# Kernel tuning notes

Measured on AMD Instinct MI355X. Metric: run time of the kernel, lower is better.

Reference implementation:

```python
import jax, jax.numpy as jnp
import numpy as np

DIM = 1024
NUM_HEADS = 16
HEAD_DIM = DIM // NUM_HEADS


def setup_inputs() -> dict:
    key = jax.random.key(0)
    ks = jax.random.split(key, 9)
    s = 1.0 / np.sqrt(DIM)
    return {
        "x": jax.random.normal(ks[0], (2, 2048, DIM), dtype=jnp.float32),
        "wq": jax.random.uniform(ks[1], (DIM, DIM), jnp.float32, -s, s),
        "bq": jax.random.uniform(ks[2], (DIM,), jnp.float32, -s, s),
        "wk": jax.random.uniform(ks[3], (DIM, DIM), jnp.float32, -s, s),
        "bk": jax.random.uniform(ks[4], (DIM,), jnp.float32, -s, s),
        "wv": jax.random.uniform(ks[5], (DIM, DIM), jnp.float32, -s, s),
        "bv": jax.random.uniform(ks[6], (DIM,), jnp.float32, -s, s),
        "wo": jax.random.uniform(ks[7], (DIM, DIM), jnp.float32, -s, s),
        "bo": jax.random.uniform(ks[8], (DIM,), jnp.float32, -s, s),
    }


def reference(x, wq, bq, wk, bk, wv, bv, wo, bo):
    B, N, D = x.shape
    H, Hd = NUM_HEADS, HEAD_DIM
    # projections; weights stored as (in, out) so x @ w matches torch Linear(x) with w = W.T
    q = (x @ wq + bq).reshape(B, N, H, Hd).transpose(0, 2, 1, 3)  # [B,H,N,Hd]
    k = (x @ wk + bk).reshape(B, N, H, Hd).transpose(0, 2, 1, 3)
    v = (x @ wv + bv).reshape(B, N, H, Hd).transpose(0, 2, 1, 3)
    scale = 1.0 / np.sqrt(Hd).astype(np.float32)
    scores = jnp.einsum("bhqd,bhkd->bhqk", q, k) * scale  # [B,H,N,N]
    attn = jax.nn.softmax(scores, axis=-1)
    # dropout is identity in eval mode (reference baseline)
    out = jnp.einsum("bhqk,bhkd->bhqd", attn, v)  # [B,H,N,Hd]
    out = out.transpose(0, 2, 1, 3).reshape(B, N, D)
    return out @ wo + bo
```

## Files before the change

kernel.cpp:

```cpp
#include <hip/hip_runtime.h>

typedef __attribute__((ext_vector_type(8))) short short8;
typedef __attribute__((ext_vector_type(4))) short short4v;
typedef __attribute__((ext_vector_type(4))) float f32x4;

__device__ inline unsigned short f2bf(float f) {
  union { float f; unsigned int u; } v; v.f = f;
  unsigned int r = v.u + 0x7FFFu + ((v.u >> 16) & 1u);
  return (unsigned short)(r >> 16);
}

__device__ inline unsigned cvtpk_bf16(float lo, float hi) {
  unsigned r;
  asm("v_cvt_pk_bf16_f32 %0, %1, %2" : "=v"(r) : "v"(lo), "v"(hi));
  return r;
}

__device__ inline void gload_lds16(const void* g, void* l) {
  __builtin_amdgcn_global_load_lds(
      (const __attribute__((address_space(1))) unsigned int*)g,
      (__attribute__((address_space(3))) unsigned int*)l, 16, 0, 0);
}


__global__ __launch_bounds__(256) void prep(
    const float* __restrict__ x,
    const float* __restrict__ wq, const float* __restrict__ wk,
    const float* __restrict__ wv, const float* __restrict__ wo,
    const float* __restrict__ bq, const float* __restrict__ bk,
    const float* __restrict__ bv,
    unsigned short* __restrict__ xb, unsigned short* __restrict__ wqkvT,
    unsigned short* __restrict__ woT, float* __restrict__ bqkv) {
  const int bid = blockIdx.x;
  if (bid < 4096) {
    const int i = bid * 256 + threadIdx.x;
    float4 v = ((const float4*)x)[i];
    ushort4 o;
    o.x = f2bf(v.x); o.y = f2bf(v.y); o.z = f2bf(v.z); o.w = f2bf(v.w);
    ((ushort4*)xb)[i] = o;
  } else if (bid < 8192) {
    const int u = bid - 4096;
    const int z = u >> 10, rem = u & 1023;
    const float* w = (z == 0) ? wq : (z == 1) ? wk : (z == 2) ? wv : wo;
    unsigned short* dst = (z < 3) ? (wqkvT + (size_t)z * 1024 * 1024) : woT;
    const float scale = (z == 0) ? 0.18033688011f : 1.0f;
    __shared__ float t[32][33];
    const int k0 = (rem & 31) * 32;
    const int n0 = (rem >> 5) * 32;
    const int tx = threadIdx.x & 31, ty = threadIdx.x >> 5;
#pragma unroll
    for (int i = 0; i < 32; i += 8)
      t[ty + i][tx] = w[(size_t)(k0 + ty + i) * 1024 + n0 + tx];
    __syncthreads();
#pragma unroll
    for (int i = 0; i < 32; i += 8)
      dst[(size_t)(n0 + ty + i) * 1024 + k0 + tx] = f2bf(t[tx][ty + i] * scale);
  } else {
    const int i = (bid - 8192) * 256 + threadIdx.x;
    float v;
    if (i < 1024) v = bq[i] * 0.18033688011f;
    else if (i < 2048) v = bk[i - 1024];
    else v = bv[i - 2048];
    bqkv[i] = v;
  }
}


__global__ __launch_bounds__(256) void gemm_bt64(
    const unsigned short* __restrict__ A, const unsigned short* __restrict__ Bt,
    const float* __restrict__ bias, float* __restrict__ C, int K, int ldc) {
  __shared__ unsigned short As[64 * 32];
  __shared__ unsigned short Bs[128 * 32];
  const int tid = threadIdx.x;
  const int lane = tid & 63;
  const int wave = tid >> 6;
  const int wm = (wave >> 1) * 32;
  const int wn = (wave & 1) * 64;
  const long bm = (long)blockIdx.x * 64;
  const long bn = (long)blockIdx.y * 128;

  const int sr = tid >> 2;
  const int sc = (tid & 3) * 8;
  const unsigned short* Ag0 = A + (bm + sr) * (long)K + sc;
  const unsigned short* Bg0 = Bt + (bn + sr) * (long)K + sc;
  const unsigned short* Bg1 = Bt + (bn + 64 + sr) * (long)K + sc;
  unsigned short* As0 = &As[tid * 8];
  unsigned short* Bs0 = &Bs[tid * 8];
  unsigned short* Bs1 = &Bs[2048 + tid * 8];

  f32x4 acc[2][4] = {};

  const int fr = lane & 15;
  const int fk = (lane >> 4) * 8;

  for (int kt = 0; kt < K; kt += 32) {
    gload_lds16(Ag0, As0);
    gload_lds16(Bg0, Bs0);
    gload_lds16(Bg1, Bs1);
    Ag0 += 32; Bg0 += 32; Bg1 += 32;
    __syncthreads();
    short8 af[2], bfv[4];
#pragma unroll
    for (int i = 0; i < 2; i++) af[i] = *(const short8*)&As[(wm + i * 16 + fr) * 32 + fk];
#pragma unroll
    for (int j = 0; j < 4; j++) bfv[j] = *(const short8*)&Bs[(wn + j * 16 + fr) * 32 + fk];
#pragma unroll
    for (int i = 0; i < 2; i++)
#pragma unroll
      for (int j = 0; j < 4; j++)
        acc[i][j] = __builtin_amdgcn_mfma_f32_16x16x32_bf16(af[i], bfv[j], acc[i][j], 0, 0, 0);
    __syncthreads();
  }

  const int crow = (lane >> 4) * 4;
  const int ccol = lane & 15;
#pragma unroll
  for (int j = 0; j < 4; j++) {
    const long col = bn + wn + j * 16 + ccol;
    const float bv = bias[col];
#pragma unroll
    for (int i = 0; i < 2; i++)
#pragma unroll
      for (int r = 0; r < 4; r++) {
        const long row = bm + wm + i * 16 + crow + r;
        C[row * ldc + col] = acc[i][j][r] + bv;
      }
  }
}


__global__ __launch_bounds__(512, 2) void gemm256(
    const unsigned short* __restrict__ A, const unsigned short* __restrict__ Bt,
    const float* __restrict__ bias, unsigned short* __restrict__ C, int ldc) {
  constexpr int K = 1024;
  __shared__ unsigned short Sab[2][2][16384];
  const int tid = threadIdx.x;
  const int lane = tid & 63;
  const int w = tid >> 6;
  const int wr = w >> 2, wc = w & 3;
  const long bm = (long)blockIdx.x * 256;
  const long bn = (long)blockIdx.y * 256;
  const int fr = lane & 15, fg = lane >> 4;

  const int srow = tid >> 3;
  const int kch = tid & 7;

  auto stage = [&](int o, int buf, int tk, int h) {
#pragma unroll
    for (int l = 0; l < 2; ++l) {
      const int rih = l * 64 + srow;
      const unsigned short* src = (o ? Bt : A) +
          ((o ? bn : bm) + h * 128 + rih) * (long)K + tk * 64 + ((kch ^ (rih & 7)) * 8);
      gload_lds16(src, &Sab[buf][o][h * 8192 + (l * 512 + tid) * 8]);
    }
  };

  f32x4 acc[8][4] = {};

  stage(0, 0, 0, 0); stage(0, 0, 0, 1);
  stage(1, 0, 0, 0); stage(1, 0, 0, 1);
  stage(1, 1, 1, 0); stage(1, 1, 1, 1);
  asm volatile("s_waitcnt vmcnt(4)" ::: "memory");
  __builtin_amdgcn_s_barrier();

  for (int it = 0; it < 8; ++it) {
    const int T = 2 * it;
    const int tkA = (T + 2 < 15) ? T + 2 : 15;
    const int tkB3 = (T + 3 < 15) ? T + 3 : 15;
#pragma unroll
    for (int half = 0; half < 2; ++half) {
      const int b = half;
      short8 bfr[4][2];
      short8 afr[2][2];
#pragma unroll
      for (int g = 0; g < 4; ++g) {
        if (g == 0) {
#pragma unroll
          for (int nj = 0; nj < 4; ++nj)
#pragma unroll
            for (int kc = 0; kc < 2; ++kc) {
              const int r = wc * 64 + nj * 16 + fr;
              bfr[nj][kc] = *(const short8*)&Sab[b][1][r * 64 + ((kc * 4 + fg) ^ (r & 7)) * 8];
            }
        }
#pragma unroll
        for (int mil = 0; mil < 2; ++mil)
#pragma unroll
          for (int kc = 0; kc < 2; ++kc) {
            const int r = wr * 128 + (2 * g + mil) * 16 + fr;
            afr[mil][kc] = *(const short8*)&Sab[b][0][r * 64 + ((kc * 4 + fg) ^ (r & 7)) * 8];
          }
        if (half == 0) {
          if (g == 0)      { stage(0, 1, T + 1, 0); stage(0, 1, T + 1, 1); }
          else if (g == 1) { stage(1, 0, tkA, 0); }
          else if (g == 2) { stage(1, 0, tkA, 1); }
        } else {
          if (g == 0)      { stage(0, 0, tkA, 0); stage(0, 0, tkA, 1); }
          else if (g == 1) { stage(1, 1, tkB3, 0); }
          else if (g == 2) { stage(1, 1, tkB3, 1); }
        }
        __builtin_amdgcn_s_barrier();
        asm volatile("s_waitcnt lgkmcnt(0)" ::: "memory");
        __builtin_amdgcn_sched_barrier(0);
        __builtin_amdgcn_s_setprio(1);
#pragma unroll
        for (int mil = 0; mil < 2; ++mil)
#pragma unroll
          for (int nj = 0; nj < 4; ++nj)
#pragma unroll
            for (int kc = 0; kc < 2; ++kc)
              acc[2 * g + mil][nj] = __builtin_amdgcn_mfma_f32_16x16x32_bf16(
                  afr[mil][kc], bfr[nj][kc], acc[2 * g + mil][nj], 0, 0, 0);
        __builtin_amdgcn_s_setprio(0);
        if (g == 3) asm volatile("s_waitcnt vmcnt(4)" ::: "memory");
        __builtin_amdgcn_s_barrier();
      }
    }
  }

  const int crow = fg * 4;
  const int ccol = fr;
#pragma unroll
  for (int nj = 0; nj < 4; ++nj) {
    const long col = bn + wc * 64 + nj * 16 + ccol;
    const float bv = bias[col];
#pragma unroll
    for (int mi = 0; mi < 8; ++mi)
#pragma unroll
      for (int r = 0; r < 4; ++r) {
        const long row = bm + wr * 128 + mi * 16 + crow + r;
        C[row * ldc + col] = f2bf(acc[mi][nj][r] + bv);
      }
  }
}


#define KSWZ(row) (((row) & 3) | ((((row) >> 3) & 1) << 2))
#define TRRD(d, o) asm volatile("ds_read_b64_tr_b16 %0, %1 offset:" o \
                                : "=v"(d) : "v"(vtr) : "memory")
#define LGKM(n) asm volatile("s_waitcnt lgkmcnt(" #n ")" ::: "memory")

__global__ __launch_bounds__(256, 5) void attn_fwd(
    const unsigned short* __restrict__ qkv, unsigned short* __restrict__ out) {
  __shared__ unsigned short Ks[2 * 4096];
  __shared__ unsigned short Vs[2 * 4096];
  const int tid = threadIdx.x;
  const int lane = tid & 63;
  const int w = tid >> 6;
  const int qh = w >> 1, kh = w & 1;

  const int xcd = blockIdx.x & 7, slot = blockIdx.x >> 3;
  const int pair = xcd * 4 + (slot >> 5);
  const int qtile = slot & 31;
  const int h = pair & 15, b = pair >> 4;
  const long rowbase = (long)b * 2048;
  const int hq = h * 64;
  const int fr = lane & 15;
  const int fg = lane >> 4;
  const int fk = fg * 8;
  const int q0 = qtile * 64 + qh * 32;

  short8 qf[2][2];
#pragma unroll
  for (int qi = 0; qi < 2; qi++) {
    const long qr = rowbase + q0 + qi * 16 + fr;
    qf[qi][0] = *(const short8*)&qkv[qr * 3072 + hq + fk];
    qf[qi][1] = *(const short8*)&qkv[qr * 3072 + hq + 32 + fk];
  }

  const int kr0 = tid >> 3, kr1 = 32 + (tid >> 3);
  const unsigned short* Kg0 = &qkv[(rowbase + kr0) * 3072 + 1024 + hq + (((tid & 7) ^ KSWZ(kr0)) * 8)];
  const unsigned short* Kg1 = &qkv[(rowbase + kr1) * 3072 + 1024 + hq + (((tid & 7) ^ KSWZ(kr1)) * 8)];
  const int vkv0 = ((tid >> 3) & 3) * 8 + ((tid >> 5) & 1) * 4 + ((tid >> 1) & 3);
  const int vd0 = ((tid >> 6) & 3) * 16 + (tid & 1) * 8;
  const unsigned short* Vg0 = &qkv[(rowbase + vkv0) * 3072 + 2048 + hq + vd0];
  const unsigned short* Vg1 = &qkv[(rowbase + vkv0 + 32) * 3072 + 2048 + hq + vd0];

  auto stage = [&](int buf) {
    gload_lds16(Kg0, &Ks[buf * 4096 + tid * 8]);
    gload_lds16(Kg1, &Ks[buf * 4096 + 2048 + tid * 8]);
    gload_lds16(Vg0, &Vs[buf * 4096 + tid * 8]);
    gload_lds16(Vg1, &Vs[buf * 4096 + 2048 + tid * 8]);
    Kg0 += 64 * 3072; Kg1 += 64 * 3072; Vg0 += 64 * 3072; Vg1 += 64 * 3072;
  };

  f32x4 o[2][4] = {};
  float m_[2] = {-1e30f, -1e30f};
  float s_[2] = {0.f, 0.f};

  const int krowbase = kh * 32 + (fr >> 2) * 8 + (fr & 3);

  stage(0);
  __syncthreads();

  for (int t = 0; t < 32; t++) {
    const int cur = t & 1;
    if (t < 31) stage(cur ^ 1);

    f32x4 sa[2][2];
    __builtin_amdgcn_s_setprio(1);
#pragma unroll
    for (int n = 0; n < 2; n++) {
      const int row = krowbase + n * 4;
      const short8 kf0 = *(const short8*)&Ks[cur * 4096 + ((row * 64 + fk) ^ (KSWZ(row) << 3))];
      const short8 kf1 = *(const short8*)&Ks[cur * 4096 + ((row * 64 + 32 + fk) ^ (KSWZ(row) << 3))];
#pragma unroll
      for (int qi = 0; qi < 2; qi++) {
        f32x4 z = {0.f, 0.f, 0.f, 0.f};
        z = __builtin_amdgcn_mfma_f32_16x16x32_bf16(kf0, qf[qi][0], z, 0, 0, 0);
        sa[qi][n] = __builtin_amdgcn_mfma_f32_16x16x32_bf16(kf1, qf[qi][1], z, 0, 0, 0);
      }
    }
    __builtin_amdgcn_s_setprio(0);

    float lmax[2];
#pragma unroll
    for (int qi = 0; qi < 2; qi++)
      lmax[qi] = fmaxf(fmaxf(fmaxf(sa[qi][0][0], sa[qi][0][1]), fmaxf(sa[qi][0][2], sa[qi][0][3])),
                       fmaxf(fmaxf(sa[qi][1][0], sa[qi][1][1]), fmaxf(sa[qi][1][2], sa[qi][1][3])));
    if (__any(fmaxf(lmax[0] - m_[0], lmax[1] - m_[1]) > 8.f)) {
#pragma unroll
      for (int qi = 0; qi < 2; qi++) {
        float mx = lmax[qi];
        mx = fmaxf(mx, __shfl_xor(mx, 16));
        mx = fmaxf(mx, __shfl_xor(mx, 32));
        const float nm = fmaxf(m_[qi], mx);
        const float fac = __builtin_amdgcn_exp2f(m_[qi] - nm);
        m_[qi] = nm;
        s_[qi] *= fac;
        float facp[4];
#pragma unroll
        for (int r = 0; r < 4; r++) facp[r] = __shfl(fac, fg * 4 + r);
#pragma unroll
        for (int dj = 0; dj < 4; dj++)
#pragma unroll
          for (int r = 0; r < 4; r++) o[qi][dj][r] *= facp[r];
      }
    }

    short8 pa[2];
#pragma unroll
    for (int qi = 0; qi < 2; qi++) {
      float p[8];
#pragma unroll
      for (int n = 0; n < 2; n++)
#pragma unroll
        for (int r = 0; r < 4; r++)
          p[n * 4 + r] = __builtin_amdgcn_exp2f(sa[qi][n][r] - m_[qi]);
      float sl = ((p[0] + p[1]) + (p[2] + p[3])) + ((p[4] + p[5]) + (p[6] + p[7]));
      sl += __shfl_xor(sl, 16);
      sl += __shfl_xor(sl, 32);
      s_[qi] += sl;
      union { unsigned u[4]; short8 v; } pk;
      pk.u[0] = cvtpk_bf16(p[0], p[1]);
      pk.u[1] = cvtpk_bf16(p[2], p[3]);
      pk.u[2] = cvtpk_bf16(p[4], p[5]);
      pk.u[3] = cvtpk_bf16(p[6], p[7]);
      pa[qi] = pk.v;
    }

    const __attribute__((address_space(3))) unsigned short* vtr =
        (const __attribute__((address_space(3))) unsigned short*)&Vs[0] +
        cur * 4096 + kh * 2048 + lane * 4;
    short4v v0[4], v1[4];
    TRRD(v0[0], "0");    TRRD(v1[0], "512");
    TRRD(v0[1], "1024"); TRRD(v1[1], "1536");
    TRRD(v0[2], "2048"); TRRD(v1[2], "2560");
    TRRD(v0[3], "3072"); TRRD(v1[3], "3584");

    __builtin_amdgcn_s_setprio(1);
    LGKM(6); __builtin_amdgcn_sched_barrier(0);
    {
      short8 vf = __builtin_shufflevector(v0[0], v1[0], 0, 1, 2, 3, 4, 5, 6, 7);
      o[0][0] = __builtin_amdgcn_mfma_f32_16x16x32_bf16(pa[0], vf, o[0][0], 0, 0, 0);
      o[1][0] = __builtin_amdgcn_mfma_f32_16x16x32_bf16(pa[1], vf, o[1][0], 0, 0, 0);
    }
    LGKM(4); __builtin_amdgcn_sched_barrier(0);
    {
      short8 vf = __builtin_shufflevector(v0[1], v1[1], 0, 1, 2, 3, 4, 5, 6, 7);
      o[0][1] = __builtin_amdgcn_mfma_f32_16x16x32_bf16(pa[0], vf, o[0][1], 0, 0, 0);
      o[1][1] = __builtin_amdgcn_mfma_f32_16x16x32_bf16(pa[1], vf, o[1][1], 0, 0, 0);
    }
    LGKM(2); __builtin_amdgcn_sched_barrier(0);
    {
      short8 vf = __builtin_shufflevector(v0[2], v1[2], 0, 1, 2, 3, 4, 5, 6, 7);
      o[0][2] = __builtin_amdgcn_mfma_f32_16x16x32_bf16(pa[0], vf, o[0][2], 0, 0, 0);
      o[1][2] = __builtin_amdgcn_mfma_f32_16x16x32_bf16(pa[1], vf, o[1][2], 0, 0, 0);
    }
    LGKM(0); __builtin_amdgcn_sched_barrier(0);
    {
      short8 vf = __builtin_shufflevector(v0[3], v1[3], 0, 1, 2, 3, 4, 5, 6, 7);
      o[0][3] = __builtin_amdgcn_mfma_f32_16x16x32_bf16(pa[0], vf, o[0][3], 0, 0, 0);
      o[1][3] = __builtin_amdgcn_mfma_f32_16x16x32_bf16(pa[1], vf, o[1][3], 0, 0, 0);
    }
    __builtin_amdgcn_s_setprio(0);
    __syncthreads();
  }

  float* mo = (float*)&Ks[0];
  float* ms = (float*)&Vs[0];
  __syncthreads();
  if (kh == 1) {
#pragma unroll
    for (int qi = 0; qi < 2; qi++)
#pragma unroll
      for (int dj = 0; dj < 4; dj++)
#pragma unroll
        for (int r = 0; r < 4; r++)
          mo[(qh * 32 + qi * 16 + dj * 4 + r) * 64 + lane] = o[qi][dj][r];
  }
  if (fg == 0) {
#pragma unroll
    for (int qi = 0; qi < 2; qi++) {
      ms[(((kh * 2 + qh) * 2 + qi) * 2 + 0) * 16 + fr] = m_[qi];
      ms[(((kh * 2 + qh) * 2 + qi) * 2 + 1) * 16 + fr] = s_[qi];
    }
  }
  __syncthreads();
  if (kh == 0) {
#pragma unroll
    for (int qi = 0; qi < 2; qi++) {
      float f0[4], f1[4], rs[4];
#pragma unroll
      for (int r = 0; r < 4; r++) {
        const int qp = fg * 4 + r;
        const float m0 = ms[(((0 * 2 + qh) * 2 + qi) * 2 + 0) * 16 + qp];
        const float s0 = ms[(((0 * 2 + qh) * 2 + qi) * 2 + 1) * 16 + qp];
        const float m1 = ms[(((1 * 2 + qh) * 2 + qi) * 2 + 0) * 16 + qp];
        const float s1 = ms[(((1 * 2 + qh) * 2 + qi) * 2 + 1) * 16 + qp];
        const float mstar = fmaxf(m0, m1);
        f0[r] = __builtin_amdgcn_exp2f(m0 - mstar);
        f1[r] = __builtin_amdgcn_exp2f(m1 - mstar);
        rs[r] = __builtin_amdgcn_rcpf(s0 * f0[r] + s1 * f1[r]);
      }
#pragma unroll
      for (int dj = 0; dj < 4; dj++)
#pragma unroll
        for (int r = 0; r < 4; r++) {
          const float o1 = mo[(qh * 32 + qi * 16 + dj * 4 + r) * 64 + lane];
          const float val = (o[qi][dj][r] * f0[r] + o1 * f1[r]) * rs[r];
          const long row = rowbase + q0 + qi * 16 + fg * 4 + r;
          out[row * 1024 + hq + dj * 16 + fr] = f2bf(val);
        }
    }
  }
}


extern "C" void kernel_launch(void* const* d_in, const int* in_sizes, int n_in,
                              void* d_out, int out_size, void* d_ws, size_t ws_size,
                              hipStream_t stream) {
  const float* x  = (const float*)d_in[0];
  const float* wq = (const float*)d_in[1];
  const float* bq = (const float*)d_in[2];
  const float* wk = (const float*)d_in[3];
  const float* bk = (const float*)d_in[4];
  const float* wv = (const float*)d_in[5];
  const float* bv = (const float*)d_in[6];
  const float* wo = (const float*)d_in[7];
  const float* bo = (const float*)d_in[8];

  char* ws = (char*)d_ws;
  unsigned short* xb    = (unsigned short*)(ws);
  unsigned short* wqkvT = (unsigned short*)(ws + (8ull  << 20));
  unsigned short* woT   = (unsigned short*)(ws + (14ull << 20));
  float*          bqkv  = (float*)         (ws + (16ull << 20));
  unsigned short* qkv   = (unsigned short*)(ws + (17ull << 20));
  unsigned short* attn  = (unsigned short*)(ws + (41ull << 20));

  prep<<<8204, 256, 0, stream>>>(x, wq, wk, wv, wo, bq, bk, bv, xb, wqkvT, woT, bqkv);

  gemm256<<<dim3(16, 12), 512, 0, stream>>>(xb, wqkvT, bqkv, qkv, 3072);

  attn_fwd<<<1024, 256, 0, stream>>>(qkv, attn);

  gemm_bt64<<<dim3(64, 8), 256, 0, stream>>>(attn, woT, bo, (float*)d_out, 1024, 1024);
}
```

Before: 123.6 us.

## Double attention block size to 128 query rows with 512 threads sharing K/V tiles

The attention kernel now uses 512 threads per block covering 128 query rows instead of 256 threads covering 64, and launches half as many blocks. Each K/V tile staged into LDS is shared by twice as many query rows, which halves global/L2 traffic for K and V, and each thread issues one K and one V load per stage instead of two. The softmax max/sum merge moves to a dedicated shared array sized for eight warps. The costs are fewer blocks in flight (512 over the device), lower occupancy bounds, and more waves contending at each barrier.

```diff
diff --git a/kernel.cpp b/kernel.cpp
--- a/kernel.cpp
+++ b/kernel.cpp
@@ -240,25 +240,27 @@
                                 : "=v"(d) : "v"(vtr) : "memory")
 #define LGKM(n) asm volatile("s_waitcnt lgkmcnt(" #n ")" ::: "memory")
 
-__global__ __launch_bounds__(256, 5) void attn_fwd(
+__global__ __launch_bounds__(512, 4) void attn_fwd(
     const unsigned short* __restrict__ qkv, unsigned short* __restrict__ out) {
-  __shared__ unsigned short Ks[2 * 4096];
-  __shared__ unsigned short Vs[2 * 4096];
+  __shared__ unsigned short S[4 * 4096];
+  __shared__ float msArr[512];
+  unsigned short* Ks = &S[0];
+  unsigned short* Vs = &S[8192];
   const int tid = threadIdx.x;
   const int lane = tid & 63;
   const int w = tid >> 6;
   const int qh = w >> 1, kh = w & 1;
 
   const int xcd = blockIdx.x & 7, slot = blockIdx.x >> 3;
-  const int pair = xcd * 4 + (slot >> 5);
-  const int qtile = slot & 31;
+  const int pair = xcd * 4 + (slot >> 4);
+  const int qtile = slot & 15;
   const int h = pair & 15, b = pair >> 4;
   const long rowbase = (long)b * 2048;
   const int hq = h * 64;
   const int fr = lane & 15;
   const int fg = lane >> 4;
   const int fk = fg * 8;
-  const int q0 = qtile * 64 + qh * 32;
+  const int q0 = qtile * 128 + qh * 32;
 
   short8 qf[2][2];
 #pragma unroll
@@ -268,20 +270,16 @@
     qf[qi][1] = *(const short8*)&qkv[qr * 3072 + hq + 32 + fk];
   }
 
-  const int kr0 = tid >> 3, kr1 = 32 + (tid >> 3);
-  const unsigned short* Kg0 = &qkv[(rowbase + kr0) * 3072 + 1024 + hq + (((tid & 7) ^ KSWZ(kr0)) * 8)];
-  const unsigned short* Kg1 = &qkv[(rowbase + kr1) * 3072 + 1024 + hq + (((tid & 7) ^ KSWZ(kr1)) * 8)];
-  const int vkv0 = ((tid >> 3) & 3) * 8 + ((tid >> 5) & 1) * 4 + ((tid >> 1) & 3);
-  const int vd0 = ((tid >> 6) & 3) * 16 + (tid & 1) * 8;
-  const unsigned short* Vg0 = &qkv[(rowbase + vkv0) * 3072 + 2048 + hq + vd0];
-  const unsigned short* Vg1 = &qkv[(rowbase + vkv0 + 32) * 3072 + 2048 + hq + vd0];
+  const int kr = tid >> 3;
+  const unsigned short* Kg = &qkv[(rowbase + kr) * 3072 + 1024 + hq + (((tid & 7) ^ KSWZ(kr)) * 8)];
+  const int vkv = ((tid >> 1) & 3) + ((tid >> 5) & 1) * 4 + ((tid >> 3) & 3) * 8 + ((tid >> 8) & 1) * 32;
+  const int vd0 = (tid & 1) * 8 + ((tid >> 6) & 3) * 16;
+  const unsigned short* Vg = &qkv[(rowbase + vkv) * 3072 + 2048 + hq + vd0];
 
   auto stage = [&](int buf) {
-    gload_lds16(Kg0, &Ks[buf * 4096 + tid * 8]);
-    gload_lds16(Kg1, &Ks[buf * 4096 + 2048 + tid * 8]);
-    gload_lds16(Vg0, &Vs[buf * 4096 + tid * 8]);
-    gload_lds16(Vg1, &Vs[buf * 4096 + 2048 + tid * 8]);
-    Kg0 += 64 * 3072; Kg1 += 64 * 3072; Vg0 += 64 * 3072; Vg1 += 64 * 3072;
+    gload_lds16(Kg, &Ks[buf * 4096 + tid * 8]);
+    gload_lds16(Vg, &Vs[buf * 4096 + tid * 8]);
+    Kg += 64 * 3072; Vg += 64 * 3072;
   };
 
   f32x4 o[2][4] = {};
@@ -397,8 +395,7 @@
     __syncthreads();
   }
 
-  float* mo = (float*)&Ks[0];
-  float* ms = (float*)&Vs[0];
+  float* mo = (float*)&S[0];
   __syncthreads();
   if (kh == 1) {
 #pragma unroll
@@ -412,8 +409,8 @@
   if (fg == 0) {
 #pragma unroll
     for (int qi = 0; qi < 2; qi++) {
-      ms[(((kh * 2 + qh) * 2 + qi) * 2 + 0) * 16 + fr] = m_[qi];
-      ms[(((kh * 2 + qh) * 2 + qi) * 2 + 1) * 16 + fr] = s_[qi];
+      msArr[(((kh * 4 + qh) * 2 + qi) * 2 + 0) * 16 + fr] = m_[qi];
+      msArr[(((kh * 4 + qh) * 2 + qi) * 2 + 1) * 16 + fr] = s_[qi];
     }
   }
   __syncthreads();
@@ -424,10 +421,10 @@
 #pragma unroll
       for (int r = 0; r < 4; r++) {
         const int qp = fg * 4 + r;
-        const float m0 = ms[(((0 * 2 + qh) * 2 + qi) * 2 + 0) * 16 + qp];
-        const float s0 = ms[(((0 * 2 + qh) * 2 + qi) * 2 + 1) * 16 + qp];
-        const float m1 = ms[(((1 * 2 + qh) * 2 + qi) * 2 + 0) * 16 + qp];
-        const float s1 = ms[(((1 * 2 + qh) * 2 + qi) * 2 + 1) * 16 + qp];
+        const float m0 = msArr[(((0 * 4 + qh) * 2 + qi) * 2 + 0) * 16 + qp];
+        const float s0 = msArr[(((0 * 4 + qh) * 2 + qi) * 2 + 1) * 16 + qp];
+        const float m1 = msArr[(((1 * 4 + qh) * 2 + qi) * 2 + 0) * 16 + qp];
+        const float s1 = msArr[(((1 * 4 + qh) * 2 + qi) * 2 + 1) * 16 + qp];
         const float mstar = fmaxf(m0, m1);
         f0[r] = __builtin_amdgcn_exp2f(m0 - mstar);
         f1[r] = __builtin_amdgcn_exp2f(m1 - mstar);
@@ -472,7 +469,7 @@
 
   gemm256<<<dim3(16, 12), 512, 0, stream>>>(xb, wqkvT, bqkv, qkv, 3072);
 
-  attn_fwd<<<1024, 256, 0, stream>>>(qkv, attn);
+  attn_fwd<<<512, 512, 0, stream>>>(qkv, attn);
 
   gemm_bt64<<<dim3(64, 8), 256, 0, stream>>>(attn, woT, bo, (float*)d_out, 1024, 1024);
 }
```

Result: faster. 118.0 us (-4.5%).
